# Performance work log

Hardware: AMD Instinct MI355X
Metric: run time of the kernel (lower is better)

## Reference

```python
import jax, jax.numpy as jnp
import numpy as np

V, E, H, TAG, B, S = 100000, 128, 256, 16, 64, 512
T = TAG + 2            # tag_size + start + end
START, END = T - 2, T - 1


def setup_inputs() -> dict:
    key = jax.random.key(0)
    ks = jax.random.split(key, 16)
    x = jax.random.randint(ks[0], (B, S), 0, V)
    lengths = jax.random.randint(ks[1], (B,), S // 2, S + 1)
    mask = (jnp.arange(S)[None, :] < lengths[:, None]).astype(jnp.int32)

    def rn(k, shape, s=0.05):
        return (jax.random.normal(k, shape) * s).astype(jnp.float32)

    embed = rn(ks[2], (V, E), 0.1)
    Wih_f = rn(ks[3], (4 * H, E)); Whh_f = rn(ks[4], (4 * H, H))
    bih_f = rn(ks[5], (4 * H,));   bhh_f = rn(ks[6], (4 * H,))
    Wih_b = rn(ks[7], (4 * H, E)); Whh_b = rn(ks[8], (4 * H, H))
    bih_b = rn(ks[9], (4 * H,));   bhh_b = rn(ks[10], (4 * H,))
    Wc = rn(ks[11], (T, 2 * H));   bc = rn(ks[12], (T,))
    trans = rn(ks[13], (T, T), 0.1)
    trans = trans.at[:, START].set(-1000.0).at[END, :].set(-1000.0)
    h0 = rn(ks[14], (2, B, H), 1.0)  # init_hidden uses randn
    c0 = rn(ks[15], (2, B, H), 1.0)
    return dict(x=x, mask=mask, embed=embed,
                Wih_f=Wih_f, Whh_f=Whh_f, bih_f=bih_f, bhh_f=bhh_f,
                Wih_b=Wih_b, Whh_b=Whh_b, bih_b=bih_b, bhh_b=bhh_b,
                Wc=Wc, bc=bc, trans=trans, h0=h0, c0=c0)


def _lstm_dir(xs, h0, c0, Wih, Whh, bih, bhh, reverse):
    # xs: [S,B,E]; PyTorch gate order i,f,g,o
    xp = jnp.einsum('sbe,ge->sbg', xs, Wih) + bih  # batch the input GEMM

    def step(carry, xg):
        h, c = carry
        g = xg + h @ Whh.T + bhh
        i, f, gg, o = jnp.split(g, 4, axis=-1)
        c = jax.nn.sigmoid(f) * c + jax.nn.sigmoid(i) * jnp.tanh(gg)
        h = jax.nn.sigmoid(o) * jnp.tanh(c)
        return (h, c), h

    _, hs = jax.lax.scan(step, (h0, c0), xp, reverse=reverse)
    return hs  # [S,B,H]


def _viterbi(feats, mask, trans):
    # feats [B,S,T]; scores[t,b,prev,cur] = feats[t,b,cur] + trans[prev,cur]
    scores = feats.transpose(1, 0, 2)[:, :, None, :] + trans[None, None, :, :]  # [S,B,T,T]
    mT = mask.T  # [S,B]
    partition0 = scores[0, :, START, :]  # [B,T]

    def step(partition, inp):
        sc_t, m_t = inp
        cur = sc_t + partition[:, :, None]        # add over prev-tag axis
        new_p = jnp.max(cur, axis=1)
        bp = jnp.argmax(cur, axis=1).astype(jnp.int32)
        bp = jnp.where(m_t[:, None] > 0, bp, 0)   # zero back-pointers at pad
        return new_p, (new_p, bp)

    _, (parts, bps) = jax.lax.scan(step, partition0, (scores[1:], mT[1:]))
    part_hist = jnp.concatenate([partition0[None], parts], axis=0)  # [S,B,T]

    lengths = jnp.sum(mask, axis=1)
    last_pos = lengths - 1  # [B]
    ph_b = part_hist.transpose(1, 0, 2)  # [B,S,T]
    last_part = jnp.take_along_axis(ph_b, last_pos[:, None, None], axis=1)[:, 0, :]  # [B,T]
    last_vals = last_part[:, :, None] + trans[None]
    max_value = jnp.max(last_vals, axis=1)                    # [B,T]
    last_bp = jnp.argmax(last_vals, axis=1).astype(jnp.int32)
    pointer = last_bp[:, END]                                  # [B]

    back = jnp.concatenate([bps, jnp.zeros((1, B, T), jnp.int32)], axis=0)  # [S,B,T]
    bp_b = back.transpose(1, 0, 2)  # [B,S,T]
    bp_b = bp_b.at[jnp.arange(B), last_pos].set(pointer[:, None])  # insert_last scatter
    back = bp_b.transpose(1, 0, 2)

    def trace(ptr, bp_t):
        new = jnp.take_along_axis(bp_t, ptr[:, None], axis=1)[:, 0]
        return new, new

    _, dec = jax.lax.scan(trace, pointer, back[:-1], reverse=True)  # [S-1,B]
    decode = jnp.concatenate([dec, pointer[None]], axis=0).T        # [B,S]
    path_score = max_value[:, END]
    return path_score, decode


def reference(x, mask, embed, Wih_f, Whh_f, bih_f, bhh_f,
              Wih_b, Whh_b, bih_b, bhh_b, Wc, bc, trans, h0, c0):
    xs = embed[x].transpose(1, 0, 2)  # [S,B,E]
    hf = _lstm_dir(xs, h0[0], c0[0], Wih_f, Whh_f, bih_f, bhh_f, False)
    hb = _lstm_dir(xs, h0[1], c0[1], Wih_b, Whh_b, bih_b, bhh_b, True)
    out = jnp.concatenate([hf, hb], axis=-1)            # [S,B,2H]
    feats = (out @ Wc.T + bc).transpose(1, 0, 2)        # [B,S,T]
    return _viterbi(feats, mask, trans)
```

## Files before the change

### kernel.cpp

```cpp
#include <hip/hip_runtime.h>

#define SLEN 512
#define BATCH 64
#define HID 256
#define EMB 128
#define NT 18
#define NCHAIN 128
#define FB 8
#define SB 16

typedef unsigned int u32;

__device__ __forceinline__ float sigmoidf_(float v) { return 1.0f / (1.0f + expf(-v)); }
__device__ __forceinline__ u32 aload(const u32* p) {
  return __hip_atomic_load((u32*)p, __ATOMIC_RELAXED, __HIP_MEMORY_SCOPE_AGENT);
}
__device__ __forceinline__ void bar() {
  __builtin_amdgcn_sched_barrier(0);
  asm volatile("s_waitcnt lgkmcnt(0)" ::: "memory");
  __builtin_amdgcn_s_barrier();
  __builtin_amdgcn_sched_barrier(0);
}

__global__ __launch_bounds__(512, 2) void lstm_kernel(
    const int* __restrict__ x, const float* __restrict__ embed,
    const float* __restrict__ Wih_f, const float* __restrict__ Whh_f,
    const float* __restrict__ bih_f, const float* __restrict__ bhh_f,
    const float* __restrict__ Wih_b, const float* __restrict__ Whh_b,
    const float* __restrict__ bih_b, const float* __restrict__ bhh_b,
    const float* __restrict__ h0, const float* __restrict__ c0,
    float* __restrict__ h_hist, u32* __restrict__ flags)
{
  const int rk   = blockIdx.x >> 6;
  const int q    = blockIdx.x & 63;
  const int dir  = q >> 5;
  const int bA   = (q & 31) * 2, bB = bA + 1;
  const int chA  = dir * BATCH + bA, chB = chA + 1;
  const int tid  = threadIdx.x;
  const int wv   = tid >> 6;
  const int lane = tid & 63;
  const int rb   = lane * 4;
  const int gi   = rb >> 6;
  const int grow0 = gi * 256 + rk * 64 + (rb & 63);

  const float* Wih = dir ? Wih_b : Wih_f;
  const float* Whh = dir ? Whh_b : Whh_f;
  const float* bih = dir ? bih_b : bih_f;
  const float* bhh = dir ? bhh_b : bhh_f;

  float4 wreg[4][12];
#pragma unroll
  for (int i = 0; i < 4; ++i)
#pragma unroll
    for (int c = 0; c < 12; ++c) {
      int k0 = wv * 48 + c * 4;
      if (k0 < 256)
        wreg[i][c] = *(const float4*)(Whh + (size_t)(grow0 + i) * 256 + k0);
      else
        wreg[i][c] = *(const float4*)(Wih + (size_t)(grow0 + i) * 128 + (k0 - 256));
    }

  __shared__ float vA[384], vB[384];
  __shared__ float redA[8 * 256], redB[8 * 256];

  float bias4[4] = {0, 0, 0, 0};
  float creg = 0.0f;
  if (wv >= 6) {
    int b = (wv == 6) ? bA : bB;
#pragma unroll
    for (int gg = 0; gg < 4; ++gg)
      bias4[gg] = bih[gg * 256 + rk * 64 + lane] + bhh[gg * 256 + rk * 64 + lane];
    creg = c0[(size_t)(dir * BATCH + b) * HID + rk * 64 + lane];
  }

  auto TS = [&](int s) { s = s < SLEN ? s : SLEN - 1; return dir ? (SLEN - 1 - s) : s; };

  const int ee = tid - 256;
  float evA = 0.0f, evB = 0.0f;
  int xvA = 0, xvB = 0;
  u32 hwB = 0;

  if (tid < 256) {
    vA[tid] = h0[(size_t)(dir * BATCH + bA) * HID + tid];
    vB[tid] = h0[(size_t)(dir * BATCH + bB) * HID + tid];
  } else if (tid < 384) {
    vA[256 + ee] = embed[(size_t)x[bA * SLEN + TS(0)] * EMB + ee];
    evA = embed[(size_t)x[bA * SLEN + TS(1)] * EMB + ee];
    xvA = x[bA * SLEN + TS(2)];
    evB = embed[(size_t)x[bB * SLEN + TS(0)] * EMB + ee];
    xvB = x[bB * SLEN + TS(1)];
  }
  __syncthreads();

  for (int it = 0; it < SLEN; ++it) {
    const int t = dir ? (SLEN - 1 - it) : it;
    const int kb = wv * 48;

    {
      float4 acc = {0, 0, 0, 0};
#pragma unroll
      for (int c = 0; c < 12; ++c) {
        float4 v4 = *(const float4*)&vA[kb + c * 4];
        acc.x = fmaf(wreg[0][c].x, v4.x, acc.x); acc.x = fmaf(wreg[0][c].y, v4.y, acc.x);
        acc.x = fmaf(wreg[0][c].z, v4.z, acc.x); acc.x = fmaf(wreg[0][c].w, v4.w, acc.x);
        acc.y = fmaf(wreg[1][c].x, v4.x, acc.y); acc.y = fmaf(wreg[1][c].y, v4.y, acc.y);
        acc.y = fmaf(wreg[1][c].z, v4.z, acc.y); acc.y = fmaf(wreg[1][c].w, v4.w, acc.y);
        acc.z = fmaf(wreg[2][c].x, v4.x, acc.z); acc.z = fmaf(wreg[2][c].y, v4.y, acc.z);
        acc.z = fmaf(wreg[2][c].z, v4.z, acc.z); acc.z = fmaf(wreg[2][c].w, v4.w, acc.z);
        acc.w = fmaf(wreg[3][c].x, v4.x, acc.w); acc.w = fmaf(wreg[3][c].y, v4.y, acc.w);
        acc.w = fmaf(wreg[3][c].z, v4.z, acc.w); acc.w = fmaf(wreg[3][c].w, v4.w, acc.w);
      }
      *(float4*)&redA[wv * 256 + rb] = acc;
    }
    bar();

    if (wv == 6) {
      float s0 = bias4[0], s1 = bias4[1], s2 = bias4[2], s3 = bias4[3];
#pragma unroll
      for (int w = 0; w < 8; ++w) {
        s0 += redA[w * 256 + lane];
        s1 += redA[w * 256 + 64 + lane];
        s2 += redA[w * 256 + 128 + lane];
        s3 += redA[w * 256 + 192 + lane];
      }
      float ig = sigmoidf_(s0), fg = sigmoidf_(s1);
      float gv = tanhf(s2),     og = sigmoidf_(s3);
      creg = fg * creg + ig * gv;
      float hv = og * tanhf(creg);
      __hip_atomic_store(h_hist + ((size_t)(dir * SLEN + t) * BATCH + bA) * HID
                           + rk * 64 + lane,
                         hv, __ATOMIC_RELAXED, __HIP_MEMORY_SCOPE_AGENT);
      asm volatile("s_waitcnt vmcnt(0)" ::: "memory");
      if (lane == 0)
        __hip_atomic_store(flags + ((size_t)chA * SLEN + it) * 4 + rk, 1u,
                           __ATOMIC_RELAXED, __HIP_MEMORY_SCOPE_AGENT);
    } else if (tid < 256) {
      if (it > 0) *(u32*)&vB[tid] = hwB;
    } else if (wv < 6) {
      vB[256 + ee] = evB;
      evB = embed[(size_t)xvB * EMB + ee];
      xvB = x[bB * SLEN + TS(it + 2)];
    }
    bar();

    {
      float4 acc = {0, 0, 0, 0};
#pragma unroll
      for (int c = 0; c < 12; ++c) {
        float4 v4 = *(const float4*)&vB[kb + c * 4];
        acc.x = fmaf(wreg[0][c].x, v4.x, acc.x); acc.x = fmaf(wreg[0][c].y, v4.y, acc.x);
        acc.x = fmaf(wreg[0][c].z, v4.z, acc.x); acc.x = fmaf(wreg[0][c].w, v4.w, acc.x);
        acc.y = fmaf(wreg[1][c].x, v4.x, acc.y); acc.y = fmaf(wreg[1][c].y, v4.y, acc.y);
        acc.y = fmaf(wreg[1][c].z, v4.z, acc.y); acc.y = fmaf(wreg[1][c].w, v4.w, acc.y);
        acc.z = fmaf(wreg[2][c].x, v4.x, acc.z); acc.z = fmaf(wreg[2][c].y, v4.y, acc.z);
        acc.z = fmaf(wreg[2][c].z, v4.z, acc.z); acc.z = fmaf(wreg[2][c].w, v4.w, acc.z);
        acc.w = fmaf(wreg[3][c].x, v4.x, acc.w); acc.w = fmaf(wreg[3][c].y, v4.y, acc.w);
        acc.w = fmaf(wreg[3][c].z, v4.z, acc.w); acc.w = fmaf(wreg[3][c].w, v4.w, acc.w);
      }
      *(float4*)&redB[wv * 256 + rb] = acc;
    }
    bar();

    if (wv == 7) {
      float s0 = bias4[0], s1 = bias4[1], s2 = bias4[2], s3 = bias4[3];
#pragma unroll
      for (int w = 0; w < 8; ++w) {
        s0 += redB[w * 256 + lane];
        s1 += redB[w * 256 + 64 + lane];
        s2 += redB[w * 256 + 128 + lane];
        s3 += redB[w * 256 + 192 + lane];
      }
      float ig = sigmoidf_(s0), fg = sigmoidf_(s1);
      float gv = tanhf(s2),     og = sigmoidf_(s3);
      creg = fg * creg + ig * gv;
      float hv = og * tanhf(creg);
      __hip_atomic_store(h_hist + ((size_t)(dir * SLEN + t) * BATCH + bB) * HID
                           + rk * 64 + lane,
                         hv, __ATOMIC_RELAXED, __HIP_MEMORY_SCOPE_AGENT);
      asm volatile("s_waitcnt vmcnt(0)" ::: "memory");
      if (lane == 0)
        __hip_atomic_store(flags + ((size_t)chB * SLEN + it) * 4 + rk, 1u,
                           __ATOMIC_RELAXED, __HIP_MEMORY_SCOPE_AGENT);
    } else if (tid < 256) {
      if (it < SLEN - 1) {
        const u32* fpA = flags + ((size_t)chA * SLEN + it) * 4 + wv;
        u32 v = aload(fpA); int sp = 0;
        while (v == 0 && ++sp < (1 << 14)) { __builtin_amdgcn_s_sleep(1); v = aload(fpA); }
        asm volatile("" ::: "memory");
        u32 ha = aload((const u32*)(h_hist +
                   ((size_t)(dir * SLEN + t) * BATCH + bA) * HID) + tid);
        *(u32*)&vA[tid] = ha;
        const u32* fpB = flags + ((size_t)chB * SLEN + it) * 4 + wv;
        v = aload(fpB); sp = 0;
        while (v == 0 && ++sp < (1 << 14)) { __builtin_amdgcn_s_sleep(1); v = aload(fpB); }
        asm volatile("" ::: "memory");
        hwB = aload((const u32*)(h_hist +
                 ((size_t)(dir * SLEN + t) * BATCH + bB) * HID) + tid);
      }
    } else if (wv < 6) {
      if (it < SLEN - 1) {
        vA[256 + ee] = evA;
        evA = embed[(size_t)xvA * EMB + ee];
        xvA = x[bA * SLEN + TS(it + 3)];
      }
    }
    bar();
  }
}

__global__ __launch_bounds__(256) void feats_kernel(
    const float* __restrict__ h_hist, const float* __restrict__ Wc,
    const float* __restrict__ bc, float* __restrict__ feats)
{
  const int s0  = (blockIdx.x >> 3) * SB;
  const int b0  = (blockIdx.x & 7) * FB;
  const int tid = threadIdx.x;
  __shared__ float wc[NT * 516];
  __shared__ float hl[FB * 516];
  __shared__ float bcl[NT];
  if (tid < NT) bcl[tid] = bc[tid];
  for (int f = tid * 4; f < NT * 512; f += 1024) {
    float4 v = *(const float4*)(Wc + f);
    *(float4*)&wc[(f >> 9) * 516 + (f & 511)] = v;
  }
  for (int si = 0; si < SB; ++si) {
    const int s = s0 + si;
    const float* src0 = h_hist + ((size_t)s * BATCH + b0) * HID;
    const float* src1 = h_hist + ((size_t)(SLEN + s) * BATCH + b0) * HID;
    for (int f = tid * 4; f < FB * 256; f += 1024) {
      int b = f >> 8, j = f & 255;
      *(float4*)&hl[b * 516 + j]       = *(const float4*)(src0 + f);
      *(float4*)&hl[b * 516 + 256 + j] = *(const float4*)(src1 + f);
    }
    __syncthreads();
    if (tid < FB * NT) {
      int b = tid / NT, tag = tid - b * NT;
      float a = bcl[tag];
      const float* hp = &hl[b * 516];
      const float* wp = &wc[tag * 516];
#pragma unroll 8
      for (int k = 0; k < 512; k += 4) {
        float4 h4 = *(const float4*)(hp + k);
        float4 w4 = *(const float4*)(wp + k);
        a = fmaf(h4.x, w4.x, a); a = fmaf(h4.y, w4.y, a);
        a = fmaf(h4.z, w4.z, a); a = fmaf(h4.w, w4.w, a);
      }
      feats[((size_t)s * BATCH + b0 + b) * NT + tag] = a;
    }
    __syncthreads();
  }
}

__global__ __launch_bounds__(64) void viterbi_kernel(
    const float* __restrict__ feats, const int* __restrict__ mask,
    const float* __restrict__ trans, float* __restrict__ out)
{
  const int b = blockIdx.x;
  const int lane = threadIdx.x;
  __shared__ float flds[SLEN * NT];
  __shared__ float tr[NT][NT + 1];
  __shared__ float part[2][NT + 2];
  __shared__ float lastp[NT + 2];
  __shared__ unsigned char bp[SLEN][20];
  __shared__ int len_s;

  for (int f = lane; f < SLEN * NT; f += 64) {
    int s = f / NT, tag = f - s * NT;
    flds[f] = feats[((size_t)s * BATCH + b) * NT + tag];
  }
  for (int f = lane; f < NT * NT; f += 64) tr[f / NT][f % NT] = trans[f];
  int m = 0;
#pragma unroll
  for (int i = 0; i < 8; ++i) m += mask[b * SLEN + lane * 8 + i];
  for (int off = 32; off; off >>= 1) m += __shfl_down(m, off);
  if (lane == 0) len_s = m;
  __syncthreads();
  const int len = len_s;

  if (lane < NT) part[0][lane] = flds[lane] + tr[16][lane];
  __syncthreads();

  int cur = 0;
  for (int t = 1; t < SLEN; ++t) {
    if (lane < NT) {
      float fcur = flds[t * NT + lane];
      float best = -3.0e38f; int bf = 0;
#pragma unroll
      for (int from = 0; from < NT; ++from) {
        float v = (fcur + tr[from][lane]) + part[cur][from];
        if (v > best) { best = v; bf = from; }
      }
      part[cur ^ 1][lane] = best;
      bp[t][lane] = (t < len) ? (unsigned char)bf : (unsigned char)0;
      if (t == len - 1) lastp[lane] = best;
    }
    cur ^= 1;
    __syncthreads();
  }

  if (lane == 0) {
    float best = -3.0e38f; int bf = 0;
    for (int from = 0; from < NT; ++from) {
      float v = lastp[from] + tr[from][17];
      if (v > best) { best = v; bf = from; }
    }
    out[b] = best;
    int ptr = bf;
    out[BATCH + (size_t)b * SLEN + (SLEN - 1)] = (float)ptr;
    for (int i = SLEN - 2; i >= 0; --i) {
      int nw = (i == len - 1) ? bf : (int)bp[i + 1][ptr];
      out[BATCH + (size_t)b * SLEN + i] = (float)nw;
      ptr = nw;
    }
  }
}

extern "C" void kernel_launch(void* const* d_in, const int* in_sizes, int n_in,
                              void* d_out, int out_size, void* d_ws, size_t ws_size,
                              hipStream_t stream) {
  const int*   x      = (const int*)  d_in[0];
  const int*   mask   = (const int*)  d_in[1];
  const float* embed  = (const float*)d_in[2];
  const float* Wih_f  = (const float*)d_in[3];
  const float* Whh_f  = (const float*)d_in[4];
  const float* bih_f  = (const float*)d_in[5];
  const float* bhh_f  = (const float*)d_in[6];
  const float* Wih_b  = (const float*)d_in[7];
  const float* Whh_b  = (const float*)d_in[8];
  const float* bih_b  = (const float*)d_in[9];
  const float* bhh_b  = (const float*)d_in[10];
  const float* Wc     = (const float*)d_in[11];
  const float* bc     = (const float*)d_in[12];
  const float* trans  = (const float*)d_in[13];
  const float* h0     = (const float*)d_in[14];
  const float* c0     = (const float*)d_in[15];
  float* out = (float*)d_out;

  char* ws = (char*)d_ws;
  float* h_hist = (float*)ws;
  u32*   flags  = (u32*)(ws + (size_t)67108864);
  float* feats  = (float*)(ws + (size_t)67108864);

  hipMemsetAsync(flags, 0, (size_t)NCHAIN * SLEN * 4 * sizeof(u32), stream);
  lstm_kernel<<<256, 512, 0, stream>>>(x, embed, Wih_f, Whh_f, bih_f, bhh_f,
                                       Wih_b, Whh_b, bih_b, bhh_b, h0, c0,
                                       h_hist, flags);
  feats_kernel<<<(SLEN / SB) * 8, 256, 0, stream>>>(h_hist, Wc, bc, feats);
  viterbi_kernel<<<BATCH, 64, 0, stream>>>(feats, mask, trans, out);
}
```

Baseline: 2.013 ms.

## Interleave four batch chains per LSTM block to hide cross-block sync latency

Each persistent LSTM block now handles four batch chains instead of two, rotating GEMM phases across them, and the grid is halved to 128 blocks. This gives each chain's cross-block flag wait and h reload three other chains' worth of GEMM work to hide behind. The flag publish is deferred by one phase and the flag is pre-loaded before the GEMM so that polling usually finds it already set. The reduction buffer is shared across chains. The trade-off is half as many blocks and more serial GEMM work per block, so each step's critical path gets longer.

```diff
diff --git a/kernel.cpp b/kernel.cpp
--- a/kernel.cpp
+++ b/kernel.cpp
@@ -31,11 +31,12 @@
     const float* __restrict__ h0, const float* __restrict__ c0,
     float* __restrict__ h_hist, u32* __restrict__ flags)
 {
-  const int rk   = blockIdx.x >> 6;
-  const int q    = blockIdx.x & 63;
-  const int dir  = q >> 5;
-  const int bA   = (q & 31) * 2, bB = bA + 1;
-  const int chA  = dir * BATCH + bA, chB = chA + 1;
+  const int rk   = blockIdx.x >> 5;
+  const int q    = blockIdx.x & 31;
+  const int dir  = q >> 4;
+  const int b0   = (q & 15) * 4;
+  const int bA = b0, bB = b0 + 1, bC = b0 + 2, bD = b0 + 3;
+  const int chA = dir * BATCH + bA, chB = chA + 1, chC = chA + 2, chD = chA + 3;
   const int tid  = threadIdx.x;
   const int wv   = tid >> 6;
   const int lane = tid & 63;
@@ -59,14 +60,15 @@
       else
         wreg[i][c] = *(const float4*)(Wih + (size_t)(grow0 + i) * 128 + (k0 - 256));
     }
-
-  __shared__ float vA[384], vB[384];
-  __shared__ float redA[8 * 256], redB[8 * 256];
+  const int kb = wv * 48;
+
+  __shared__ float vA[384], vB[384], vC[384], vD[384];
+  __shared__ float red[8 * 256];
 
   float bias4[4] = {0, 0, 0, 0};
   float creg = 0.0f;
-  if (wv >= 6) {
-    int b = (wv == 6) ? bA : bB;
+  if (wv >= 4) {
+    int b = b0 + (wv - 4);
 #pragma unroll
     for (int gg = 0; gg < 4; ++gg)
       bias4[gg] = bih[gg * 256 + rk * 64 + lane] + bhh[gg * 256 + rk * 64 + lane];
@@ -75,137 +77,155 @@
 
   auto TS = [&](int s) { s = s < SLEN ? s : SLEN - 1; return dir ? (SLEN - 1 - s) : s; };
 
-  const int ee = tid - 256;
-  float evA = 0.0f, evB = 0.0f;
-  int xvA = 0, xvB = 0;
-  u32 hwB = 0;
+  float evA = 0, evB = 0, evC = 0, evD = 0;
+  int xvA = 0, xvB = 0, xvC = 0, xvD = 0;
+  u32 hwA = 0, hwB = 0, hwC = 0, hwD = 0;
 
   if (tid < 256) {
     vA[tid] = h0[(size_t)(dir * BATCH + bA) * HID + tid];
     vB[tid] = h0[(size_t)(dir * BATCH + bB) * HID + tid];
-  } else if (tid < 384) {
-    vA[256 + ee] = embed[(size_t)x[bA * SLEN + TS(0)] * EMB + ee];
-    evA = embed[(size_t)x[bA * SLEN + TS(1)] * EMB + ee];
-    xvA = x[bA * SLEN + TS(2)];
-    evB = embed[(size_t)x[bB * SLEN + TS(0)] * EMB + ee];
-    xvB = x[bB * SLEN + TS(1)];
+    vC[tid] = h0[(size_t)(dir * BATCH + bC) * HID + tid];
+    vD[tid] = h0[(size_t)(dir * BATCH + bD) * HID + tid];
+  }
+  if (tid < 128) {
+    vA[256 + tid] = embed[(size_t)x[bA * SLEN + TS(0)] * EMB + tid];
+    evB = embed[(size_t)x[bB * SLEN + TS(0)] * EMB + tid]; xvB = x[bB * SLEN + TS(1)];
+    evC = embed[(size_t)x[bC * SLEN + TS(0)] * EMB + tid]; xvC = x[bC * SLEN + TS(1)];
+    evD = embed[(size_t)x[bD * SLEN + TS(0)] * EMB + tid]; xvD = x[bD * SLEN + TS(1)];
+    evA = embed[(size_t)x[bA * SLEN + TS(1)] * EMB + tid]; xvA = x[bA * SLEN + TS(2)];
   }
   __syncthreads();
 
+#define GEMM_PHASE(VV)                                                         \
+  {                                                                            \
+    float4 acc = {0, 0, 0, 0};                                                 \
+    _Pragma("unroll")                                                          \
+    for (int c = 0; c < 12; ++c) {                                             \
+      float4 v4 = *(const float4*)&VV[kb + c * 4];                             \
+      acc.x = fmaf(wreg[0][c].x, v4.x, acc.x); acc.x = fmaf(wreg[0][c].y, v4.y, acc.x); \
+      acc.x = fmaf(wreg[0][c].z, v4.z, acc.x); acc.x = fmaf(wreg[0][c].w, v4.w, acc.x); \
+      acc.y = fmaf(wreg[1][c].x, v4.x, acc.y); acc.y = fmaf(wreg[1][c].y, v4.y, acc.y); \
+      acc.y = fmaf(wreg[1][c].z, v4.z, acc.y); acc.y = fmaf(wreg[1][c].w, v4.w, acc.y); \
+      acc.z = fmaf(wreg[2][c].x, v4.x, acc.z); acc.z = fmaf(wreg[2][c].y, v4.y, acc.z); \
+      acc.z = fmaf(wreg[2][c].z, v4.z, acc.z); acc.z = fmaf(wreg[2][c].w, v4.w, acc.z); \
+      acc.w = fmaf(wreg[3][c].x, v4.x, acc.w); acc.w = fmaf(wreg[3][c].y, v4.y, acc.w); \
+      acc.w = fmaf(wreg[3][c].z, v4.z, acc.w); acc.w = fmaf(wreg[3][c].w, v4.w, acc.w); \
+    }                                                                          \
+    *(float4*)&red[wv * 256 + rb] = acc;                                       \
+  }
+
+#define GATES(BX)                                                              \
+  {                                                                            \
+    float s0 = bias4[0], s1 = bias4[1], s2 = bias4[2], s3 = bias4[3];          \
+    _Pragma("unroll")                                                          \
+    for (int w = 0; w < 8; ++w) {                                              \
+      s0 += red[w * 256 + lane];                                               \
+      s1 += red[w * 256 + 64 + lane];                                          \
+      s2 += red[w * 256 + 128 + lane];                                         \
+      s3 += red[w * 256 + 192 + lane];                                         \
+    }                                                                          \
+    float ig = sigmoidf_(s0), fg = sigmoidf_(s1);                              \
+    float gv = tanhf(s2), og = sigmoidf_(s3);                                  \
+    creg = fg * creg + ig * gv;                                                \
+    float hv = og * tanhf(creg);                                               \
+    __hip_atomic_store(h_hist + ((size_t)(dir * SLEN + t) * BATCH + (BX)) * HID \
+                         + rk * 64 + lane,                                     \
+                       hv, __ATOMIC_RELAXED, __HIP_MEMORY_SCOPE_AGENT);        \
+  }
+
+#define PUBLISH(CH, ITX)                                                       \
+  {                                                                            \
+    asm volatile("s_waitcnt vmcnt(0)" ::: "memory");                           \
+    if (lane == 0)                                                             \
+      __hip_atomic_store(flags + ((size_t)(CH) * SLEN + (ITX)) * 4 + rk, 1u,   \
+                         __ATOMIC_RELAXED, __HIP_MEMORY_SCOPE_AGENT);          \
+  }
+
+#define POLLCHK(PV, CH, ITX, BX, TPX, HW)                                      \
+  {                                                                            \
+    if (PV == 0) {                                                             \
+      const u32* fp = flags + ((size_t)(CH) * SLEN + (ITX)) * 4 + wv;          \
+      int sp = 0; u32 v = aload(fp);                                           \
+      while (v == 0 && ++sp < (1 << 14)) { __builtin_amdgcn_s_sleep(1); v = aload(fp); } \
+    }                                                                          \
+    asm volatile("" ::: "memory");                                             \
+    HW = aload((const u32*)(h_hist +                                           \
+          ((size_t)(dir * SLEN + (TPX)) * BATCH + (BX)) * HID) + tid);         \
+  }
+
+#define EMBSTAGE(VV, EV, XV, BX, NEXTS)                                        \
+  {                                                                            \
+    VV[256 + tid] = EV;                                                        \
+    EV = embed[(size_t)(XV) * EMB + tid];                                      \
+    XV = x[(BX) * SLEN + TS(NEXTS)];                                           \
+  }
+
   for (int it = 0; it < SLEN; ++it) {
-    const int t = dir ? (SLEN - 1 - it) : it;
-    const int kb = wv * 48;
-
-    {
-      float4 acc = {0, 0, 0, 0};
-#pragma unroll
-      for (int c = 0; c < 12; ++c) {
-        float4 v4 = *(const float4*)&vA[kb + c * 4];
-        acc.x = fmaf(wreg[0][c].x, v4.x, acc.x); acc.x = fmaf(wreg[0][c].y, v4.y, acc.x);
-        acc.x = fmaf(wreg[0][c].z, v4.z, acc.x); acc.x = fmaf(wreg[0][c].w, v4.w, acc.x);
-        acc.y = fmaf(wreg[1][c].x, v4.x, acc.y); acc.y = fmaf(wreg[1][c].y, v4.y, acc.y);
-        acc.y = fmaf(wreg[1][c].z, v4.z, acc.y); acc.y = fmaf(wreg[1][c].w, v4.w, acc.y);
-        acc.z = fmaf(wreg[2][c].x, v4.x, acc.z); acc.z = fmaf(wreg[2][c].y, v4.y, acc.z);
-        acc.z = fmaf(wreg[2][c].z, v4.z, acc.z); acc.z = fmaf(wreg[2][c].w, v4.w, acc.z);
-        acc.w = fmaf(wreg[3][c].x, v4.x, acc.w); acc.w = fmaf(wreg[3][c].y, v4.y, acc.w);
-        acc.w = fmaf(wreg[3][c].z, v4.z, acc.w); acc.w = fmaf(wreg[3][c].w, v4.w, acc.w);
-      }
-      *(float4*)&redA[wv * 256 + rb] = acc;
-    }
-    bar();
-
-    if (wv == 6) {
-      float s0 = bias4[0], s1 = bias4[1], s2 = bias4[2], s3 = bias4[3];
-#pragma unroll
-      for (int w = 0; w < 8; ++w) {
-        s0 += redA[w * 256 + lane];
-        s1 += redA[w * 256 + 64 + lane];
-        s2 += redA[w * 256 + 128 + lane];
-        s3 += redA[w * 256 + 192 + lane];
-      }
-      float ig = sigmoidf_(s0), fg = sigmoidf_(s1);
-      float gv = tanhf(s2),     og = sigmoidf_(s3);
-      creg = fg * creg + ig * gv;
-      float hv = og * tanhf(creg);
-      __hip_atomic_store(h_hist + ((size_t)(dir * SLEN + t) * BATCH + bA) * HID
-                           + rk * 64 + lane,
-                         hv, __ATOMIC_RELAXED, __HIP_MEMORY_SCOPE_AGENT);
-      asm volatile("s_waitcnt vmcnt(0)" ::: "memory");
-      if (lane == 0)
-        __hip_atomic_store(flags + ((size_t)chA * SLEN + it) * 4 + rk, 1u,
-                           __ATOMIC_RELAXED, __HIP_MEMORY_SCOPE_AGENT);
-    } else if (tid < 256) {
-      if (it > 0) *(u32*)&vB[tid] = hwB;
-    } else if (wv < 6) {
-      vB[256 + ee] = evB;
-      evB = embed[(size_t)xvB * EMB + ee];
-      xvB = x[bB * SLEN + TS(it + 2)];
-    }
-    bar();
-
-    {
-      float4 acc = {0, 0, 0, 0};
-#pragma unroll
-      for (int c = 0; c < 12; ++c) {
-        float4 v4 = *(const float4*)&vB[kb + c * 4];
-        acc.x = fmaf(wreg[0][c].x, v4.x, acc.x); acc.x = fmaf(wreg[0][c].y, v4.y, acc.x);
-        acc.x = fmaf(wreg[0][c].z, v4.z, acc.x); acc.x = fmaf(wreg[0][c].w, v4.w, acc.x);
-        acc.y = fmaf(wreg[1][c].x, v4.x, acc.y); acc.y = fmaf(wreg[1][c].y, v4.y, acc.y);
-        acc.y = fmaf(wreg[1][c].z, v4.z, acc.y); acc.y = fmaf(wreg[1][c].w, v4.w, acc.y);
-        acc.z = fmaf(wreg[2][c].x, v4.x, acc.z); acc.z = fmaf(wreg[2][c].y, v4.y, acc.z);
-        acc.z = fmaf(wreg[2][c].z, v4.z, acc.z); acc.z = fmaf(wreg[2][c].w, v4.w, acc.z);
-        acc.w = fmaf(wreg[3][c].x, v4.x, acc.w); acc.w = fmaf(wreg[3][c].y, v4.y, acc.w);
-        acc.w = fmaf(wreg[3][c].z, v4.z, acc.w); acc.w = fmaf(wreg[3][c].w, v4.w, acc.w);
-      }
-      *(float4*)&redB[wv * 256 + rb] = acc;
-    }
-    bar();
-
-    if (wv == 7) {
-      float s0 = bias4[0], s1 = bias4[1], s2 = bias4[2], s3 = bias4[3];
-#pragma unroll
-      for (int w = 0; w < 8; ++w) {
-        s0 += redB[w * 256 + lane];
-        s1 += redB[w * 256 + 64 + lane];
-        s2 += redB[w * 256 + 128 + lane];
-        s3 += redB[w * 256 + 192 + lane];
-      }
-      float ig = sigmoidf_(s0), fg = sigmoidf_(s1);
-      float gv = tanhf(s2),     og = sigmoidf_(s3);
-      creg = fg * creg + ig * gv;
-      float hv = og * tanhf(creg);
-      __hip_atomic_store(h_hist + ((size_t)(dir * SLEN + t) * BATCH + bB) * HID
-                           + rk * 64 + lane,
-                         hv, __ATOMIC_RELAXED, __HIP_MEMORY_SCOPE_AGENT);
-      asm volatile("s_waitcnt vmcnt(0)" ::: "memory");
-      if (lane == 0)
-        __hip_atomic_store(flags + ((size_t)chB * SLEN + it) * 4 + rk, 1u,
-                           __ATOMIC_RELAXED, __HIP_MEMORY_SCOPE_AGENT);
-    } else if (tid < 256) {
-      if (it < SLEN - 1) {
-        const u32* fpA = flags + ((size_t)chA * SLEN + it) * 4 + wv;
-        u32 v = aload(fpA); int sp = 0;
-        while (v == 0 && ++sp < (1 << 14)) { __builtin_amdgcn_s_sleep(1); v = aload(fpA); }
-        asm volatile("" ::: "memory");
-        u32 ha = aload((const u32*)(h_hist +
-                   ((size_t)(dir * SLEN + t) * BATCH + bA) * HID) + tid);
-        *(u32*)&vA[tid] = ha;
-        const u32* fpB = flags + ((size_t)chB * SLEN + it) * 4 + wv;
-        v = aload(fpB); sp = 0;
-        while (v == 0 && ++sp < (1 << 14)) { __builtin_amdgcn_s_sleep(1); v = aload(fpB); }
-        asm volatile("" ::: "memory");
-        hwB = aload((const u32*)(h_hist +
-                 ((size_t)(dir * SLEN + t) * BATCH + bB) * HID) + tid);
-      }
-    } else if (wv < 6) {
-      if (it < SLEN - 1) {
-        vA[256 + ee] = evA;
-        evA = embed[(size_t)xvA * EMB + ee];
-        xvA = x[bA * SLEN + TS(it + 3)];
-      }
-    }
-    bar();
-  }
+    const int t  = dir ? (SLEN - 1 - it) : it;
+    const int tp = dir ? (t + 1) : (t - 1);
+    u32 pv;
+
+    if (wv == 7 && it > 0) PUBLISH(chD, it - 1)
+    pv = 1;
+    if (wv < 4 && it > 0) pv = aload(flags + ((size_t)chC * SLEN + (it - 1)) * 4 + wv);
+    __builtin_amdgcn_sched_barrier(0);
+    GEMM_PHASE(vA)
+    bar();
+    if (wv == 4) { GATES(bA) }
+    else if (wv < 4) {
+      if (it > 0) { *(u32*)&vB[tid] = hwB; }
+      if (it > 0) POLLCHK(pv, chC, it - 1, bC, tp, hwC)
+      if (tid < 128) EMBSTAGE(vB, evB, xvB, bB, it + 2)
+    }
+    bar();
+
+    if (wv == 4) PUBLISH(chA, it)
+    pv = 1;
+    if (wv < 4 && it > 0) pv = aload(flags + ((size_t)chD * SLEN + (it - 1)) * 4 + wv);
+    __builtin_amdgcn_sched_barrier(0);
+    GEMM_PHASE(vB)
+    bar();
+    if (wv == 5) { GATES(bB) }
+    else if (wv < 4) {
+      if (it > 0) { *(u32*)&vC[tid] = hwC; }
+      if (it > 0) POLLCHK(pv, chD, it - 1, bD, tp, hwD)
+      if (tid < 128) EMBSTAGE(vC, evC, xvC, bC, it + 2)
+    }
+    bar();
+
+    if (wv == 5) PUBLISH(chB, it)
+    pv = 1;
+    if (wv < 4 && it < SLEN - 1) pv = aload(flags + ((size_t)chA * SLEN + it) * 4 + wv);
+    __builtin_amdgcn_sched_barrier(0);
+    GEMM_PHASE(vC)
+    bar();
+    if (wv == 6) { GATES(bC) }
+    else if (wv < 4) {
+      if (it > 0) { *(u32*)&vD[tid] = hwD; }
+      if (it < SLEN - 1) POLLCHK(pv, chA, it, bA, t, hwA)
+      if (tid < 128) EMBSTAGE(vD, evD, xvD, bD, it + 2)
+    }
+    bar();
+
+    if (wv == 6) PUBLISH(chC, it)
+    pv = 1;
+    if (wv < 4 && it < SLEN - 1) pv = aload(flags + ((size_t)chB * SLEN + it) * 4 + wv);
+    __builtin_amdgcn_sched_barrier(0);
+    GEMM_PHASE(vD)
+    bar();
+    if (wv == 7) { GATES(bD) }
+    else if (wv < 4) {
+      if (it < SLEN - 1) { *(u32*)&vA[tid] = hwA; }
+      if (it < SLEN - 1) POLLCHK(pv, chB, it, bB, t, hwB)
+      if (tid < 128) EMBSTAGE(vA, evA, xvA, bA, it + 3)
+    }
+    bar();
+  }
+#undef GEMM_PHASE
+#undef GATES
+#undef PUBLISH
+#undef POLLCHK
+#undef EMBSTAGE
 }
 
 __global__ __launch_bounds__(256) void feats_kernel(
@@ -342,7 +362,7 @@
   float* feats  = (float*)(ws + (size_t)67108864);
 
   hipMemsetAsync(flags, 0, (size_t)NCHAIN * SLEN * 4 * sizeof(u32), stream);
-  lstm_kernel<<<256, 512, 0, stream>>>(x, embed, Wih_f, Whh_f, bih_f, bhh_f,
+  lstm_kernel<<<128, 512, 0, stream>>>(x, embed, Wih_f, Whh_f, bih_f, bhh_f,
                                        Wih_b, Whh_b, bih_b, bhh_b, h0, c0,
                                        h_hist, flags);
   feats_kernel<<<(SLEN / SB) * 8, 256, 0, stream>>>(h_hist, Wc, bc, feats);
```

Result: slower. 3.426 ms (+70.2%).
